# Kernel optimization log

Hardware: AMD Instinct MI355X
Metric: run time of the kernel (lower is better)

Reference implementation:

```python
import jax, jax.numpy as jnp
import numpy as np

B, N, H, NHEADS, N_COE, N_SCALES, THRE = 8, 1024, 128, 4, 50, 4, 5.0


def _layernorm(x, g, b, eps=1e-5):
    mu = x.mean(-1, keepdims=True)
    var = ((x - mu) ** 2).mean(-1, keepdims=True)
    return (x - mu) / jnp.sqrt(var + eps) * g + b


def setup_inputs() -> dict:
    key = jax.random.key(0)
    ks = jax.random.split(key, 12)

    def lin(k, out_d, in_d):
        lim = 1.0 / np.sqrt(in_d)
        kw, kb = jax.random.split(k)
        W = jax.random.uniform(kw, (out_d, in_d), minval=-lim, maxval=lim, dtype=jnp.float32)
        b = jax.random.uniform(kb, (out_d,), minval=-lim, maxval=lim, dtype=jnp.float32)
        return W, b

    eigw_W, eigw_b = lin(ks[0], H, H + 1)
    qkv_W, qkv_b = lin(ks[1], 3 * H, H)
    out_W, out_b = lin(ks[2], H, H)
    ffn1_W, ffn1_b = lin(ks[3], H, H)
    ffn2_W, ffn2_b = lin(ks[4], H, H)
    dsc_W, dsc_b = lin(ks[5], N_COE, H)
    dwav_W, dwav_b = lin(ks[6], N_COE, H)
    dscl_W, dscl_b = lin(ks[7], N_SCALES, H)
    # normalized-Laplacian eigenvalues live in [0, 2]
    eigenvalue = jax.random.uniform(ks[8], (B, N), minval=0.0, maxval=2.0, dtype=jnp.float32)
    eigenvector = jax.random.normal(ks[9], (B, N, N), dtype=jnp.float32) / np.sqrt(N)
    length = jnp.full((B,), N, dtype=jnp.int32)  # full graphs -> static shapes under jit
    return dict(
        eigenvalue=eigenvalue, eigenvector=eigenvector,
        eigw_W=eigw_W, eigw_b=eigw_b,
        ln1_g=jnp.ones((H,), jnp.float32), ln1_b=jnp.zeros((H,), jnp.float32),
        qkv_W=qkv_W, qkv_b=qkv_b, out_W=out_W, out_b=out_b,
        ln2_g=jnp.ones((H,), jnp.float32), ln2_b=jnp.zeros((H,), jnp.float32),
        ffn1_W=ffn1_W, ffn1_b=ffn1_b, ffn2_W=ffn2_W, ffn2_b=ffn2_b,
        dsc_W=dsc_W, dsc_b=dsc_b, dwav_W=dwav_W, dwav_b=dwav_b,
        dscl_W=dscl_W, dscl_b=dscl_b, length=length)


def _forward(eigenvalue, eigenvector, eigw_W, eigw_b, ln1_g, ln1_b, qkv_W, qkv_b,
             out_W, out_b, ln2_g, ln2_b, ffn1_W, ffn1_b, ffn2_W, ffn2_b,
             dsc_W, dsc_b, dwav_W, dwav_b, dscl_W, dscl_b, length):
    Bn, Nn = eigenvalue.shape
    mask1d = jnp.arange(Nn)[None, :] >= length[:, None]  # [B,N] True = padding

    # ---- SineEncoding ----
    ee = eigenvalue * 100.0
    div = jnp.exp(jnp.arange(0, H, 2, dtype=jnp.float32) * (-np.log(10000.0) / H))
    pe = ee[:, :, None] * div  # [B,N,H/2]
    eeig = jnp.concatenate([eigenvalue[:, :, None], jnp.sin(pe), jnp.cos(pe)], -1)  # [B,N,H+1]
    eig = eeig @ eigw_W.T + eigw_b  # [B,N,H]

    # ---- MHA block (pre-norm, residual) ----
    x = _layernorm(eig, ln1_g, ln1_b)
    qkv = x @ qkv_W.T + qkv_b
    q, k, v = jnp.split(qkv, 3, axis=-1)
    dh = H // NHEADS
    heads = lambda t: t.reshape(Bn, Nn, NHEADS, dh).transpose(0, 2, 1, 3)
    q, k, v = heads(q), heads(k), heads(v)
    scores = jnp.einsum('bhnd,bhmd->bhnm', q, k) / np.sqrt(dh)
    scores = jnp.where(mask1d[:, None, None, :], -1e9, scores)
    attn = jax.nn.softmax(scores, axis=-1)
    o = jnp.einsum('bhnm,bhmd->bhnd', attn, v).transpose(0, 2, 1, 3).reshape(Bn, Nn, H)
    eig = eig + (o @ out_W.T + out_b)

    # ---- FFN block (pre-norm, residual) ----
    y = _layernorm(eig, ln2_g, ln2_b)
    y = jax.nn.gelu(y @ ffn1_W.T + ffn1_b, approximate=False) @ ffn2_W.T + ffn2_b
    eig = eig + y

    # ---- decoders: masked mean-pool over eigenvalue axis ----
    len_f = length.astype(eig.dtype)[:, None] + 1e-8

    def pooled(W, b):
        c = eig @ W.T + b
        c = jnp.where(mask1d[:, :, None], 0.0, c)
        return c.sum(1) / len_f

    coe_scaling = jax.nn.sigmoid(pooled(dsc_W, dsc_b))          # [B,n_coe]
    coe_scaling = coe_scaling / (coe_scaling.sum(-1, keepdims=True) + 1e-8)
    coe_wavelet = jax.nn.sigmoid(pooled(dwav_W, dwav_b))        # [B,n_coe]
    coe_wavelet = coe_wavelet / (coe_wavelet.sum(-1, keepdims=True) + 1e-8)
    coe_scales = jax.nn.sigmoid(pooled(dscl_W, dscl_b)) * THRE  # [B,n_scales]

    # ---- Chebyshev-like recurrence (gen_base) via scan ----
    def gen_base(yv):
        te0, to0 = jnp.ones_like(yv), yv
        def step(carry, _):
            te, to = carry
            te = 2.0 * yv * to - te
            to = 2.0 * yv * te - to
            return (te, to), (te, to)
        _, (evens, odds) = jax.lax.scan(step, (te0, to0), None, length=N_COE - 1)
        wav = jnp.concatenate([te0[None], evens], 0)   # [n_coe, ...]
        scal = jnp.concatenate([to0[None], odds], 0)
        return scal, wav

    base_scaling, _ = gen_base(eigenvalue[:, :, None] - 1.0)  # [n_coe,B,N,1]
    fsw = eigenvalue[:, :, None] * coe_scales[:, None, :]     # [B,N,S]
    fsw = jnp.where(fsw > 2.0, 0.0, fsw)
    _, base_wavelet = gen_base(fsw - 1.0)                     # [n_coe,B,N,S]
    base_scaling = 0.5 * (1.0 - base_scaling)
    base_wavelet = 0.5 * (1.0 - base_wavelet)

    curr_scaling = jnp.einsum('bc,cbns->bns', coe_scaling, base_scaling)  # [B,N,1]
    curr_wavelet = jnp.einsum('bc,cbns->bns', coe_wavelet, base_wavelet)  # [B,N,S]
    fsa = jnp.concatenate([curr_scaling, curr_wavelet], -1)               # [B,N,S+1]
    # tight-frame normalization (cfg.lam.tight_use = True)
    fsa = fsa / (jnp.linalg.norm(fsa, axis=-1, keepdims=True) + 1e-8)

    # filters_i = evc @ diag(fsa[:,:,i]) @ evc^T, all scales at once
    filters = jnp.einsum('bnk,bks,bmk->bsnm', eigenvector, fsa, eigenvector)
    # F.normalize(filters) with default dim=1 -> normalize over row axis (n here)
    norm = jnp.sqrt(jnp.sum(filters ** 2, axis=2, keepdims=True))
    filters = filters / jnp.maximum(norm, 1e-12)
    # filters[edge_idx] with full lengths == flatten over (B,N,N), per scale
    bases = filters.transpose(1, 0, 2, 3).reshape(N_SCALES + 1, -1)
    return bases


def reference(eigenvalue, eigenvector, eigw_W, eigw_b, ln1_g, ln1_b, qkv_W, qkv_b,
              out_W, out_b, ln2_g, ln2_b, ffn1_W, ffn1_b, ffn2_W, ffn2_b,
              dsc_W, dsc_b, dwav_W, dwav_b, dscl_W, dscl_b, length):
    return _forward(eigenvalue, eigenvector, eigw_W, eigw_b, ln1_g, ln1_b, qkv_W, qkv_b,
                    out_W, out_b, ln2_g, ln2_b, ffn1_W, ffn1_b, ffn2_W, ffn2_b,
                    dsc_W, dsc_b, dwav_W, dwav_b, dscl_W, dscl_b, length)
```

## Files before the change

kernel.cpp:

```cpp
#include <hip/hip_runtime.h>
#include <hip/hip_bf16.h>
#include <cstdint>

#define BB 8
#define NV 1024
#define HH 128
#define DH 32
#define NCOE 50
#define NSC 4

#define WOFF_EIG 0
#define WOFF_QKV 16384
#define WOFF_OUT 65536
#define WOFF_F1  81920
#define WOFF_F2  98304
#define WB_ELEMS 114688

typedef __attribute__((ext_vector_type(8))) short short8;
typedef __attribute__((ext_vector_type(4))) float f32x4;

__device__ __forceinline__ ushort f2bf(float f) {
    uint32_t x = __float_as_uint(f);
    uint32_t r = x + 0x7FFFu + ((x >> 16) & 1u);
    return (ushort)(r >> 16);
}

#define GLDS(gp, lp) __builtin_amdgcn_global_load_lds((const __attribute__((address_space(1))) void*)(gp), (__attribute__((address_space(3))) void*)(lp), 16, 0, 0)

__global__ void k_wcvt(const float* __restrict__ eigw_W, const float* __restrict__ qkv_W,
                       const float* __restrict__ out_W, const float* __restrict__ f1W,
                       const float* __restrict__ f2W, ushort* __restrict__ Wb) {
    int idx = blockIdx.x * 256 + threadIdx.x;
    float v; int dst;
    if (idx < 16384) {
        int r = idx >> 7, k = idx & 127;
        v = eigw_W[r * 129 + 1 + k];
        dst = WOFF_EIG + (k >> 5) * 4096 + r * 32 + (k & 31);
    } else if (idx < 65536) {
        int l = idx - 16384; int c = l >> 14, rem = l & 16383;
        int r = rem >> 7, k = rem & 127;
        v = qkv_W[(size_t)(c * 128 + r) * 128 + k];
        dst = WOFF_QKV + c * 16384 + (k >> 5) * 4096 + r * 32 + (k & 31);
    } else if (idx < 81920) {
        int l = idx - 65536; int r = l >> 7, k = l & 127;
        v = out_W[r * 128 + k];
        dst = WOFF_OUT + (k >> 5) * 4096 + r * 32 + (k & 31);
    } else if (idx < 98304) {
        int l = idx - 81920; int r = l >> 7, k = l & 127;
        v = f1W[r * 128 + k];
        dst = WOFF_F1 + (k >> 5) * 4096 + r * 32 + (k & 31);
    } else {
        int l = idx - 98304; int r = l >> 7, k = l & 127;
        v = f2W[r * 128 + k];
        dst = WOFF_F2 + (k >> 5) * 4096 + r * 32 + (k & 31);
    }
    Wb[dst] = f2bf(v);
}

__global__ __launch_bounds__(256) void k_enc_sine(const float* __restrict__ ev, const ushort* __restrict__ Wb,
                                                  const float* __restrict__ eigw_W, const float* __restrict__ eigw_b,
                                                  float* __restrict__ eig) {
    __shared__ ushort As[16384];
    __shared__ ushort Bs[16384];
    int row0 = blockIdx.x * 128;
    int t = threadIdx.x, lane = t & 63, w = t >> 6;
    int wr = w >> 1, wc = w & 1;
#pragma unroll
    for (int p = 0; p < 8; ++p) {
        int ci = w * 8 + p;
        GLDS(Wb + WOFF_EIG + ci * 512 + lane * 8, Bs + ci * 512);
    }
    {
        int r = t >> 1, half = t & 1;
        float e = ev[row0 + r] * 100.0f;
#pragma unroll
        for (int ch = 0; ch < 8; ++ch) {
            short8 u;
#pragma unroll
            for (int l = 0; l < 8; ++l) {
                int j = ch * 8 + l;
                float div = expf((float)(2 * j) * -0.07195578415606394f);
                float pe = e * div;
                u[l] = (short)f2bf(half ? cosf(pe) : sinf(pe));
            }
            int k = half * 64 + ch * 8;
            *(short8*)(As + (k >> 5) * 4096 + r * 32 + (k & 31)) = u;
        }
    }
    __syncthreads();
    int cl = lane & 15, q = lane >> 4;
    f32x4 acc[4][4] = {};
#pragma unroll
    for (int kt = 0; kt < 4; ++kt) {
        const ushort* ap = As + kt * 4096 + (wr * 64 + cl) * 32 + q * 8;
        const ushort* bp = Bs + kt * 4096 + (wc * 64 + cl) * 32 + q * 8;
        short8 af[4], bfr[4];
#pragma unroll
        for (int i = 0; i < 4; ++i) af[i] = *(const short8*)(ap + i * 512);
#pragma unroll
        for (int j = 0; j < 4; ++j) bfr[j] = *(const short8*)(bp + j * 512);
#pragma unroll
        for (int i = 0; i < 4; ++i)
#pragma unroll
            for (int j = 0; j < 4; ++j)
                acc[i][j] = __builtin_amdgcn_mfma_f32_16x16x32_bf16(af[i], bfr[j], acc[i][j], 0, 0, 0);
    }
#pragma unroll
    for (int i = 0; i < 4; ++i) {
        int rbase = wr * 64 + i * 16 + q * 4;
        float er[4];
#pragma unroll
        for (int r = 0; r < 4; ++r) er[r] = ev[row0 + rbase + r];
#pragma unroll
        for (int j = 0; j < 4; ++j) {
            int col = wc * 64 + j * 16 + cl;
            float w0 = eigw_W[col * 129];
            float bv = eigw_b[col];
#pragma unroll
            for (int r = 0; r < 4; ++r)
                eig[(size_t)(row0 + rbase + r) * HH + col] = acc[i][j][r] + er[r] * w0 + bv;
        }
    }
}

__global__ __launch_bounds__(256) void k_enc_qkv(const float* __restrict__ eig, const float* __restrict__ g,
                                                 const float* __restrict__ be, const ushort* __restrict__ Wb,
                                                 const float* __restrict__ bias,
                                                 ushort* __restrict__ qb, ushort* __restrict__ kb, ushort* __restrict__ vb) {
    __shared__ ushort As[16384];
    __shared__ ushort Bs[16384];
    int row0 = blockIdx.x * 128;
    int t = threadIdx.x, lane = t & 63, w = t >> 6;
    int wr = w >> 1, wc = w & 1;
    {
        int r = t >> 1, half = t & 1;
        const float4* rowp = (const float4*)(eig + (size_t)(row0 + r) * HH + half * 64);
        float4 v[16];
        float s = 0.f, s2 = 0.f;
#pragma unroll
        for (int i = 0; i < 16; ++i) {
            float4 a = rowp[i]; v[i] = a;
            s += a.x + a.y + a.z + a.w;
            s2 += a.x * a.x + a.y * a.y + a.z * a.z + a.w * a.w;
        }
        s += __shfl_xor(s, 1); s2 += __shfl_xor(s2, 1);
        float mean = s * 0.0078125f;
        float var = s2 * 0.0078125f - mean * mean;
        float rstd = rsqrtf(var + 1e-5f);
        const float4* g4 = (const float4*)(g + half * 64);
        const float4* b4 = (const float4*)(be + half * 64);
#pragma unroll
        for (int ch = 0; ch < 8; ++ch) {
            float4 a = v[2 * ch], b2 = v[2 * ch + 1];
            float4 ga = g4[2 * ch], gb = g4[2 * ch + 1];
            float4 ba = b4[2 * ch], bb = b4[2 * ch + 1];
            short8 u;
            u[0] = (short)f2bf((a.x - mean) * rstd * ga.x + ba.x);
            u[1] = (short)f2bf((a.y - mean) * rstd * ga.y + ba.y);
            u[2] = (short)f2bf((a.z - mean) * rstd * ga.z + ba.z);
            u[3] = (short)f2bf((a.w - mean) * rstd * ga.w + ba.w);
            u[4] = (short)f2bf((b2.x - mean) * rstd * gb.x + bb.x);
            u[5] = (short)f2bf((b2.y - mean) * rstd * gb.y + bb.y);
            u[6] = (short)f2bf((b2.z - mean) * rstd * gb.z + bb.z);
            u[7] = (short)f2bf((b2.w - mean) * rstd * gb.w + bb.w);
            int k = half * 64 + ch * 8;
            *(short8*)(As + (k >> 5) * 4096 + r * 32 + (k & 31)) = u;
        }
    }
    int cl = lane & 15, q = lane >> 4;
    int bidx = row0 >> 10, nbase = row0 & (NV - 1);
    ushort* dsts[3] = {qb, kb, vb};
#pragma unroll 1
    for (int c = 0; c < 3; ++c) {
        __syncthreads();
#pragma unroll
        for (int p = 0; p < 8; ++p) {
            int ci = w * 8 + p;
            GLDS(Wb + WOFF_QKV + c * 16384 + ci * 512 + lane * 8, Bs + ci * 512);
        }
        __syncthreads();
        f32x4 acc[4][4] = {};
#pragma unroll
        for (int kt = 0; kt < 4; ++kt) {
            const ushort* ap = As + kt * 4096 + (wr * 64 + cl) * 32 + q * 8;
            const ushort* bp = Bs + kt * 4096 + (wc * 64 + cl) * 32 + q * 8;
            short8 af[4], bfr[4];
#pragma unroll
            for (int i = 0; i < 4; ++i) af[i] = *(const short8*)(ap + i * 512);
#pragma unroll
            for (int j = 0; j < 4; ++j) bfr[j] = *(const short8*)(bp + j * 512);
#pragma unroll
            for (int i = 0; i < 4; ++i)
#pragma unroll
                for (int j = 0; j < 4; ++j)
                    acc[i][j] = __builtin_amdgcn_mfma_f32_16x16x32_bf16(af[i], bfr[j], acc[i][j], 0, 0, 0);
        }
        ushort* dst = dsts[c];
#pragma unroll
        for (int j = 0; j < 4; ++j) {
            int col = wc * 64 + j * 16 + cl;
            float bv = bias[c * 128 + col];
            int h = col >> 5, dd = col & 31;
            ushort* hb = dst + ((size_t)(bidx * 4 + h) * NV + nbase) * DH + dd;
#pragma unroll
            for (int i = 0; i < 4; ++i) {
                int rbase = wr * 64 + i * 16 + q * 4;
#pragma unroll
                for (int r = 0; r < 4; ++r)
                    hb[(size_t)(rbase + r) * DH] = f2bf(acc[i][j][r] + bv);
            }
        }
    }
}

__global__ __launch_bounds__(256) void k_vt(const ushort* __restrict__ vb, ushort* __restrict__ vt) {
    __shared__ ushort Ld[256 * 40];
    int bh = blockIdx.y, n0 = blockIdx.x * 256;
    int t = threadIdx.x;
    const ushort* src = vb + ((size_t)bh * NV + n0) * DH;
#pragma unroll
    for (int p = 0; p < 4; ++p) {
        int idx = p * 256 + t;
        int rowi = idx >> 2, ch = idx & 3;
        short8 u = *(const short8*)(src + idx * 8);
        *(short8*)(&Ld[rowi * 40 + ch * 8]) = u;
    }
    __syncthreads();
    int d = t >> 3, nc = (t & 7) * 32;
    ushort* dst = vt + ((size_t)bh * DH + d) * NV + n0 + nc;
#pragma unroll
    for (int p = 0; p < 4; ++p) {
        short8 u;
#pragma unroll
        for (int i = 0; i < 8; ++i) u[i] = (short)Ld[(nc + p * 8 + i) * 40 + d];
        *(short8*)(dst + p * 8) = u;
    }
}

__global__ __launch_bounds__(256) void k_qk(const ushort* __restrict__ qb, const ushort* __restrict__ kb,
                                            float* __restrict__ S) {
    __shared__ ushort As[128 * 32];
    __shared__ ushort Bs[128 * 32];
    int tile = blockIdx.x;
    int bh = blockIdx.y;
    int n0 = (tile >> 3) * 128, m0 = (tile & 7) * 128;
    int tid = threadIdx.x, lane = tid & 63, w = tid >> 6;
    int wr = w >> 1, wc = w & 1;
    const ushort* qt = qb + ((size_t)bh * NV + n0) * DH;
    const ushort* ktb = kb + ((size_t)bh * NV + m0) * DH;
#pragma unroll
    for (int p = 0; p < 2; ++p) {
        int ci = w * 2 + p;
        GLDS(qt + ci * 512 + lane * 8, As + ci * 512);
        GLDS(ktb + ci * 512 + lane * 8, Bs + ci * 512);
    }
    __syncthreads();
    int cl = lane & 15, q = lane >> 4;
    const ushort* ap = As + ((wr * 64 + cl) * 32 + q * 8);
    const ushort* bp = Bs + ((wc * 64 + cl) * 32 + q * 8);
    short8 af[4], bfr[4];
#pragma unroll
    for (int i = 0; i < 4; ++i) af[i] = *(const short8*)(ap + i * 512);
#pragma unroll
    for (int j = 0; j < 4; ++j) bfr[j] = *(const short8*)(bp + j * 512);
    f32x4 acc[4][4] = {};
#pragma unroll
    for (int i = 0; i < 4; ++i)
#pragma unroll
        for (int j = 0; j < 4; ++j)
            acc[i][j] = __builtin_amdgcn_mfma_f32_16x16x32_bf16(af[i], bfr[j], acc[i][j], 0, 0, 0);
    size_t sb = (size_t)bh * NV * NV;
#pragma unroll
    for (int i = 0; i < 4; ++i) {
        int rbase = n0 + wr * 64 + i * 16 + q * 4;
#pragma unroll
        for (int j = 0; j < 4; ++j) {
            int col = m0 + wc * 64 + j * 16 + cl;
#pragma unroll
            for (int r = 0; r < 4; ++r)
                S[sb + (size_t)(rbase + r) * NV + col] = acc[i][j][r] * 0.17677669529663687f;
        }
    }
}

__global__ __launch_bounds__(256) void k_softmax(float* __restrict__ S) {
    __shared__ float red[4];
    int row = blockIdx.x, t = threadIdx.x, lane = t & 63;
    float* rp = S + (size_t)row * NV;
    float4 v = ((const float4*)rp)[t];
    float m = fmaxf(fmaxf(v.x, v.y), fmaxf(v.z, v.w));
#pragma unroll
    for (int off = 32; off; off >>= 1) m = fmaxf(m, __shfl_xor(m, off));
    if (lane == 0) red[t >> 6] = m;
    __syncthreads();
    m = fmaxf(fmaxf(red[0], red[1]), fmaxf(red[2], red[3]));
    __syncthreads();
    float e0 = __expf(v.x - m), e1 = __expf(v.y - m), e2 = __expf(v.z - m), e3 = __expf(v.w - m);
    float s4 = e0 + e1 + e2 + e3;
#pragma unroll
    for (int off = 32; off; off >>= 1) s4 += __shfl_xor(s4, off);
    if (lane == 0) red[t >> 6] = s4;
    __syncthreads();
    float inv = 1.0f / (red[0] + red[1] + red[2] + red[3]);
    ushort4 o;
    o.x = f2bf(e0 * inv); o.y = f2bf(e1 * inv); o.z = f2bf(e2 * inv); o.w = f2bf(e3 * inv);
    ((ushort4*)rp)[t] = o;
}

__global__ __launch_bounds__(256) void k_pv(const float* __restrict__ Sf, const ushort* __restrict__ vt,
                                            ushort* __restrict__ obuf) {
    __shared__ ushort As[128 * 32];
    __shared__ ushort Bs[32 * 32];
    int n0 = blockIdx.x * 128, bh = blockIdx.y;
    int b = bh >> 2, h = bh & 3;
    int tid = threadIdx.x, lane = tid & 63, w = tid >> 6;
    const char* Sb = (const char*)Sf;
    const ushort* vtb = vt + (size_t)bh * DH * NV;
    f32x4 acc[2][2] = {};
    for (int kt = 0; kt < NV / 32; ++kt) {
        int k0 = kt * 32;
        __syncthreads();
#pragma unroll
        for (int p = 0; p < 2; ++p) {
            int ci = w * 2 + p;
            int rrow = ci * 16 + (lane >> 2);
            int kch = (lane & 3) * 8;
            const ushort* gp = (const ushort*)(Sb + (size_t)(bh * NV + n0 + rrow) * 4096) + k0 + kch;
            GLDS(gp, As + ci * 512);
        }
        if (tid < 128) {
            int d = tid >> 2, ch = tid & 3;
            short8 u = *(const short8*)(vtb + (size_t)d * NV + k0 + ch * 8);
            *(short8*)(&Bs[d * 32 + ch * 8]) = u;
        }
        __syncthreads();
        int cl = lane & 15, q = lane >> 4;
        const ushort* ap = As + ((w * 32 + cl) * 32 + q * 8);
        const ushort* bp = Bs + (cl * 32 + q * 8);
        short8 af[2], bfr[2];
#pragma unroll
        for (int i = 0; i < 2; ++i) af[i] = *(const short8*)(ap + i * 512);
#pragma unroll
        for (int j = 0; j < 2; ++j) bfr[j] = *(const short8*)(bp + j * 512);
#pragma unroll
        for (int i = 0; i < 2; ++i)
#pragma unroll
            for (int j = 0; j < 2; ++j)
                acc[i][j] = __builtin_amdgcn_mfma_f32_16x16x32_bf16(af[i], bfr[j], acc[i][j], 0, 0, 0);
    }
    int cl = lane & 15, q = lane >> 4;
#pragma unroll
    for (int i = 0; i < 2; ++i) {
        int rbase = n0 + w * 32 + i * 16 + q * 4;
#pragma unroll
        for (int j = 0; j < 2; ++j) {
            int d = j * 16 + cl;
#pragma unroll
            for (int r = 0; r < 4; ++r)
                obuf[((size_t)(b * NV + rbase + r)) * HH + h * DH + d] = f2bf(acc[i][j][r]);
        }
    }
}

__global__ __launch_bounds__(256) void k_enc_proj(const ushort* __restrict__ obuf, const ushort* __restrict__ Wb,
                                                  const float* __restrict__ bias, float* __restrict__ eig) {
    __shared__ ushort As[16384];
    __shared__ ushort Bs[16384];
    int row0 = blockIdx.x * 128;
    int t = threadIdx.x, lane = t & 63, w = t >> 6;
    int wr = w >> 1, wc = w & 1;
#pragma unroll
    for (int p = 0; p < 8; ++p) {
        int ci = w * 8 + p;
        int kt = ci >> 3, rb = ci & 7;
        const ushort* gp = obuf + (size_t)(row0 + rb * 16 + (lane >> 2)) * HH + kt * 32 + (lane & 3) * 8;
        GLDS(gp, As + kt * 4096 + rb * 512);
        GLDS(Wb + WOFF_OUT + ci * 512 + lane * 8, Bs + ci * 512);
    }
    __syncthreads();
    int cl = lane & 15, q = lane >> 4;
    f32x4 acc[4][4] = {};
#pragma unroll
    for (int kt = 0; kt < 4; ++kt) {
        const ushort* ap = As + kt * 4096 + (wr * 64 + cl) * 32 + q * 8;
        const ushort* bp = Bs + kt * 4096 + (wc * 64 + cl) * 32 + q * 8;
        short8 af[4], bfr[4];
#pragma unroll
        for (int i = 0; i < 4; ++i) af[i] = *(const short8*)(ap + i * 512);
#pragma unroll
        for (int j = 0; j < 4; ++j) bfr[j] = *(const short8*)(bp + j * 512);
#pragma unroll
        for (int i = 0; i < 4; ++i)
#pragma unroll
            for (int j = 0; j < 4; ++j)
                acc[i][j] = __builtin_amdgcn_mfma_f32_16x16x32_bf16(af[i], bfr[j], acc[i][j], 0, 0, 0);
    }
#pragma unroll
    for (int j = 0; j < 4; ++j) {
        int col = wc * 64 + j * 16 + cl;
        float bv = bias[col];
#pragma unroll
        for (int i = 0; i < 4; ++i) {
            int rbase = wr * 64 + i * 16 + q * 4;
#pragma unroll
            for (int r = 0; r < 4; ++r) {
                size_t o = (size_t)(row0 + rbase + r) * HH + col;
                eig[o] += acc[i][j][r] + bv;
            }
        }
    }
}

__global__ __launch_bounds__(256) void k_enc_ffn(float* __restrict__ eig, const float* __restrict__ g,
                                                 const float* __restrict__ be, const ushort* __restrict__ Wb,
                                                 const float* __restrict__ b1, const float* __restrict__ b2) {
    __shared__ ushort As[16384];
    __shared__ ushort Bs[16384];
    int row0 = blockIdx.x * 128;
    int t = threadIdx.x, lane = t & 63, w = t >> 6;
    int wr = w >> 1, wc = w & 1;
    {
        int r = t >> 1, half = t & 1;
        const float4* rowp = (const float4*)(eig + (size_t)(row0 + r) * HH + half * 64);
        float4 v[16];
        float s = 0.f, s2 = 0.f;
#pragma unroll
        for (int i = 0; i < 16; ++i) {
            float4 a = rowp[i]; v[i] = a;
            s += a.x + a.y + a.z + a.w;
            s2 += a.x * a.x + a.y * a.y + a.z * a.z + a.w * a.w;
        }
        s += __shfl_xor(s, 1); s2 += __shfl_xor(s2, 1);
        float mean = s * 0.0078125f;
        float var = s2 * 0.0078125f - mean * mean;
        float rstd = rsqrtf(var + 1e-5f);
        const float4* g4 = (const float4*)(g + half * 64);
        const float4* b4 = (const float4*)(be + half * 64);
#pragma unroll
        for (int ch = 0; ch < 8; ++ch) {
            float4 a = v[2 * ch], bq = v[2 * ch + 1];
            float4 ga = g4[2 * ch], gb = g4[2 * ch + 1];
            float4 ba = b4[2 * ch], bb = b4[2 * ch + 1];
            short8 u;
            u[0] = (short)f2bf((a.x - mean) * rstd * ga.x + ba.x);
            u[1] = (short)f2bf((a.y - mean) * rstd * ga.y + ba.y);
            u[2] = (short)f2bf((a.z - mean) * rstd * ga.z + ba.z);
            u[3] = (short)f2bf((a.w - mean) * rstd * ga.w + ba.w);
            u[4] = (short)f2bf((bq.x - mean) * rstd * gb.x + bb.x);
            u[5] = (short)f2bf((bq.y - mean) * rstd * gb.y + bb.y);
            u[6] = (short)f2bf((bq.z - mean) * rstd * gb.z + bb.z);
            u[7] = (short)f2bf((bq.w - mean) * rstd * gb.w + bb.w);
            int k = half * 64 + ch * 8;
            *(short8*)(As + (k >> 5) * 4096 + r * 32 + (k & 31)) = u;
        }
    }
#pragma unroll
    for (int p = 0; p < 8; ++p) {
        int ci = w * 8 + p;
        GLDS(Wb + WOFF_F1 + ci * 512 + lane * 8, Bs + ci * 512);
    }
    __syncthreads();
    int cl = lane & 15, q = lane >> 4;
    f32x4 acc[4][4] = {};
#pragma unroll
    for (int kt = 0; kt < 4; ++kt) {
        const ushort* ap = As + kt * 4096 + (wr * 64 + cl) * 32 + q * 8;
        const ushort* bp = Bs + kt * 4096 + (wc * 64 + cl) * 32 + q * 8;
        short8 af[4], bfr[4];
#pragma unroll
        for (int i = 0; i < 4; ++i) af[i] = *(const short8*)(ap + i * 512);
#pragma unroll
        for (int j = 0; j < 4; ++j) bfr[j] = *(const short8*)(bp + j * 512);
#pragma unroll
        for (int i = 0; i < 4; ++i)
#pragma unroll
            for (int j = 0; j < 4; ++j)
                acc[i][j] = __builtin_amdgcn_mfma_f32_16x16x32_bf16(af[i], bfr[j], acc[i][j], 0, 0, 0);
    }
    __syncthreads();
#pragma unroll
    for (int j = 0; j < 4; ++j) {
        int col = wc * 64 + j * 16 + cl;
        float bv = b1[col];
        int koff = (col >> 5) * 4096 + (col & 31);
#pragma unroll
        for (int i = 0; i < 4; ++i) {
            int rbase = wr * 64 + i * 16 + q * 4;
#pragma unroll
            for (int r = 0; r < 4; ++r) {
                float a = acc[i][j][r] + bv;
                float ge = 0.5f * a * (1.0f + erff(a * 0.7071067811865475f));
                As[koff + (rbase + r) * 32] = f2bf(ge);
            }
        }
    }
#pragma unroll
    for (int p = 0; p < 8; ++p) {
        int ci = w * 8 + p;
        GLDS(Wb + WOFF_F2 + ci * 512 + lane * 8, Bs + ci * 512);
    }
    __syncthreads();
    f32x4 acc2[4][4] = {};
#pragma unroll
    for (int kt = 0; kt < 4; ++kt) {
        const ushort* ap = As + kt * 4096 + (wr * 64 + cl) * 32 + q * 8;
        const ushort* bp = Bs + kt * 4096 + (wc * 64 + cl) * 32 + q * 8;
        short8 af[4], bfr[4];
#pragma unroll
        for (int i = 0; i < 4; ++i) af[i] = *(const short8*)(ap + i * 512);
#pragma unroll
        for (int j = 0; j < 4; ++j) bfr[j] = *(const short8*)(bp + j * 512);
#pragma unroll
        for (int i = 0; i < 4; ++i)
#pragma unroll
            for (int j = 0; j < 4; ++j)
                acc2[i][j] = __builtin_amdgcn_mfma_f32_16x16x32_bf16(af[i], bfr[j], acc2[i][j], 0, 0, 0);
    }
#pragma unroll
    for (int j = 0; j < 4; ++j) {
        int col = wc * 64 + j * 16 + cl;
        float bv = b2[col];
#pragma unroll
        for (int i = 0; i < 4; ++i) {
            int rbase = wr * 64 + i * 16 + q * 4;
#pragma unroll
            for (int r = 0; r < 4; ++r) {
                size_t o = (size_t)(row0 + rbase + r) * HH + col;
                eig[o] += acc2[i][j][r] + bv;
            }
        }
    }
}

__global__ __launch_bounds__(1024) void k_meanpool(const float* __restrict__ eig, float* __restrict__ me) {
    __shared__ float part[8][HH];
    int b = blockIdx.x, t = threadIdx.x;
    int col = t & 127, grp = t >> 7;
    const float* p = eig + (size_t)b * NV * HH + (size_t)grp * 128 * HH + col;
    float s = 0.f;
    for (int n = 0; n < 128; ++n) s += p[(size_t)n * HH];
    part[grp][col] = s;
    __syncthreads();
    if (t < 128) {
        float a = 0.f;
#pragma unroll
        for (int g2 = 0; g2 < 8; ++g2) a += part[g2][t];
        me[b * HH + t] = a * (1.0f / NV);
    }
}

__global__ void k_decoders(const float* __restrict__ me,
                           const float* __restrict__ dscW, const float* __restrict__ dscb,
                           const float* __restrict__ dwavW, const float* __restrict__ dwavb,
                           const float* __restrict__ dsclW, const float* __restrict__ dsclb,
                           float* __restrict__ cs, float* __restrict__ cw, float* __restrict__ csc) {
    __shared__ float m[HH];
    __shared__ float s1[NCOE], s2[NCOE];
    __shared__ float sums[2];
    int b = blockIdx.x, t = threadIdx.x;
    m[t] = me[b * HH + t];
    m[t + 64] = me[b * HH + t + 64];
    __syncthreads();
    if (t < NCOE) {
        float a = dscb[t], a2 = dwavb[t];
        const float* w1 = dscW + t * HH;
        const float* w2 = dwavW + t * HH;
        for (int j = 0; j < HH; ++j) { a += m[j] * w1[j]; a2 += m[j] * w2[j]; }
        s1[t] = 1.f / (1.f + __expf(-a));
        s2[t] = 1.f / (1.f + __expf(-a2));
    }
    if (t < NSC) {
        float a = dsclb[t];
        const float* wv = dsclW + t * HH;
        for (int j = 0; j < HH; ++j) a += m[j] * wv[j];
        csc[b * NSC + t] = 5.0f / (1.f + __expf(-a));
    }
    __syncthreads();
    if (t == 0) {
        float a = 0.f, bb = 0.f;
        for (int c = 0; c < NCOE; ++c) { a += s1[c]; bb += s2[c]; }
        sums[0] = a; sums[1] = bb;
    }
    __syncthreads();
    if (t < NCOE) {
        cs[b * NCOE + t] = s1[t] / (sums[0] + 1e-8f);
        cw[b * NCOE + t] = s2[t] / (sums[1] + 1e-8f);
    }
}

__global__ void k_fsa(const float* __restrict__ ev, const float* __restrict__ cs,
                      const float* __restrict__ cw, const float* __restrict__ csc,
                      float* __restrict__ fsaT) {
    __shared__ float lcs[NCOE], lcw[NCOE], lsc[NSC];
    int gid = blockIdx.x * 256 + threadIdx.x;
    int b = gid >> 10, n = gid & (NV - 1);
    int t = threadIdx.x;
    if (t < NCOE) { lcs[t] = cs[b * NCOE + t]; lcw[t] = cw[b * NCOE + t]; }
    if (t < NSC) lsc[t] = csc[b * NSC + t];
    __syncthreads();
    float e = ev[gid];
    float x = e - 1.0f;
    float te = 1.f, to = x;
    float a0 = lcs[0] * 0.5f * (1.f - to);
    for (int c = 1; c < NCOE; ++c) {
        te = 2.f * x * to - te;
        to = 2.f * x * te - to;
        a0 += lcs[c] * 0.5f * (1.f - to);
    }
    float aw[NSC];
#pragma unroll
    for (int s = 0; s < NSC; ++s) {
        float f = e * lsc[s];
        if (f > 2.0f) f = 0.0f;
        float y = f - 1.0f;
        float te2 = 1.f, to2 = y, a = 0.f;
        for (int c = 1; c < NCOE; ++c) {
            te2 = 2.f * y * to2 - te2;
            to2 = 2.f * y * te2 - to2;
            a += lcw[c] * 0.5f * (1.f - te2);
        }
        aw[s] = a;
    }
    float n2 = a0 * a0;
#pragma unroll
    for (int s = 0; s < NSC; ++s) n2 += aw[s] * aw[s];
    float inv = 1.f / (sqrtf(n2) + 1e-8f);
    fsaT[((size_t)b * 5 + 0) * NV + n] = a0 * inv;
#pragma unroll
    for (int s = 0; s < NSC; ++s) fsaT[((size_t)b * 5 + 1 + s) * NV + n] = aw[s] * inv;
}

__global__ void k_tobf16(const float* __restrict__ in, ushort* __restrict__ outp) {
    int i = blockIdx.x * 256 + threadIdx.x;
    const float4* p = (const float4*)in + (size_t)i * 2;
    float4 a = p[0], bq = p[1];
    uint4 r;
    r.x = (uint)f2bf(a.x) | ((uint)f2bf(a.y) << 16);
    r.y = (uint)f2bf(a.z) | ((uint)f2bf(a.w) << 16);
    r.z = (uint)f2bf(bq.x) | ((uint)f2bf(bq.y) << 16);
    r.w = (uint)f2bf(bq.z) | ((uint)f2bf(bq.w) << 16);
    ((uint4*)outp)[i] = r;
}

__global__ __launch_bounds__(256) void k_gemm(const ushort* __restrict__ Vb,
                                              const float* __restrict__ fsaT,
                                              float* __restrict__ out,
                                              float* __restrict__ cn) {
    __shared__ ushort As[128 * 32];
    __shared__ ushort Bs[128 * 32];
    int tile = blockIdx.x;
    int bsid = blockIdx.y;
    int b = bsid / 5, s = bsid % 5;
    int n0 = (tile >> 3) * 128, m0 = (tile & 7) * 128;
    int tid = threadIdx.x, lane = tid & 63, w = tid >> 6;
    int wr = w >> 1, wc = w & 1;
    const ushort* Vbase = Vb + (size_t)b * NV * NV;
    const float* fs = fsaT + ((size_t)b * 5 + s) * NV;
    f32x4 acc[4][4] = {};

    for (int kt = 0; kt < NV / 32; ++kt) {
        int k0 = kt * 32;
        __syncthreads();
#pragma unroll
        for (int p = 0; p < 2; ++p) {
            int ci = w * 2 + p;
            int rrow = ci * 16 + (lane >> 2);
            int kch = (lane & 3) * 8;
            const ushort* gp = Vbase + (size_t)(m0 + rrow) * NV + k0 + kch;
            GLDS(gp, Bs + ci * 512);
        }
#pragma unroll
        for (int p = 0; p < 2; ++p) {
            int idx = p * 256 + tid;
            int rrow = idx >> 2;
            int kch = (idx & 3) * 8;
            const ushort* gp = Vbase + (size_t)(n0 + rrow) * NV + k0 + kch;
            uint4 raw = *(const uint4*)gp;
            const float4* fp = (const float4*)(fs + k0 + kch);
            float4 f0 = fp[0], f1 = fp[1];
            float v0 = __uint_as_float(raw.x << 16) * f0.x;
            float v1 = __uint_as_float(raw.x & 0xffff0000u) * f0.y;
            float v2 = __uint_as_float(raw.y << 16) * f0.z;
            float v3 = __uint_as_float(raw.y & 0xffff0000u) * f0.w;
            float v4 = __uint_as_float(raw.z << 16) * f1.x;
            float v5 = __uint_as_float(raw.z & 0xffff0000u) * f1.y;
            float v6 = __uint_as_float(raw.w << 16) * f1.z;
            float v7 = __uint_as_float(raw.w & 0xffff0000u) * f1.w;
            uint4 rr;
            rr.x = (uint)f2bf(v0) | ((uint)f2bf(v1) << 16);
            rr.y = (uint)f2bf(v2) | ((uint)f2bf(v3) << 16);
            rr.z = (uint)f2bf(v4) | ((uint)f2bf(v5) << 16);
            rr.w = (uint)f2bf(v6) | ((uint)f2bf(v7) << 16);
            *(uint4*)(As + rrow * 32 + kch) = rr;
        }
        __syncthreads();
        int cl = lane & 15, q = lane >> 4;
        const ushort* ap = As + ((wr * 64 + cl) * 32 + q * 8);
        const ushort* bp = Bs + ((wc * 64 + cl) * 32 + q * 8);
        short8 af[4], bfr[4];
#pragma unroll
        for (int i = 0; i < 4; ++i) af[i] = *(const short8*)(ap + i * 512);
#pragma unroll
        for (int j = 0; j < 4; ++j) bfr[j] = *(const short8*)(bp + j * 512);
#pragma unroll
        for (int i = 0; i < 4; ++i)
#pragma unroll
            for (int j = 0; j < 4; ++j)
                acc[i][j] = __builtin_amdgcn_mfma_f32_16x16x32_bf16(af[i], bfr[j], acc[i][j], 0, 0, 0);
    }
    int cl = lane & 15, q = lane >> 4;
    size_t ob = (size_t)(s * BB + b) * NV * NV;
    float colss[4] = {0.f, 0.f, 0.f, 0.f};
#pragma unroll
    for (int i = 0; i < 4; ++i) {
        int rbase = n0 + wr * 64 + i * 16 + q * 4;
#pragma unroll
        for (int j = 0; j < 4; ++j) {
            int col = m0 + wc * 64 + j * 16 + cl;
#pragma unroll
            for (int r = 0; r < 4; ++r) {
                float v = acc[i][j][r];
                out[ob + (size_t)(rbase + r) * NV + col] = v;
                colss[j] += v * v;
            }
        }
    }
    float* cnb = cn + (size_t)(s * BB + b) * NV;
#pragma unroll
    for (int j = 0; j < 4; ++j) {
        float v = colss[j];
        v += __shfl_xor(v, 16);
        v += __shfl_xor(v, 32);
        if (q == 0) atomicAdd(cnb + (m0 + wc * 64 + j * 16 + cl), v);
    }
}

__global__ void k_norm(float* __restrict__ out, const float* __restrict__ cn) {
    int bid = blockIdx.x;
    int bs = bid >> 10, n = bid & (NV - 1);
    int m4 = threadIdx.x * 4;
    float4 ssv = *(const float4*)(cn + (size_t)bs * NV + m4);
    float4* p = (float4*)(out + ((size_t)bs * NV + n) * NV + m4);
    float4 v = *p;
    v.x *= 1.f / fmaxf(sqrtf(ssv.x), 1e-12f);
    v.y *= 1.f / fmaxf(sqrtf(ssv.y), 1e-12f);
    v.z *= 1.f / fmaxf(sqrtf(ssv.z), 1e-12f);
    v.w *= 1.f / fmaxf(sqrtf(ssv.w), 1e-12f);
    *p = v;
}

extern "C" void kernel_launch(void* const* d_in, const int* in_sizes, int n_in,
                              void* d_out, int out_size, void* d_ws, size_t ws_size,
                              hipStream_t stream) {
    const float* eigenvalue = (const float*)d_in[0];
    const float* eigenvector = (const float*)d_in[1];
    const float* eigw_W = (const float*)d_in[2];
    const float* eigw_b = (const float*)d_in[3];
    const float* ln1_g = (const float*)d_in[4];
    const float* ln1_b = (const float*)d_in[5];
    const float* qkv_W = (const float*)d_in[6];
    const float* qkv_b = (const float*)d_in[7];
    const float* out_W = (const float*)d_in[8];
    const float* out_b = (const float*)d_in[9];
    const float* ln2_g = (const float*)d_in[10];
    const float* ln2_b = (const float*)d_in[11];
    const float* ffn1_W = (const float*)d_in[12];
    const float* ffn1_b = (const float*)d_in[13];
    const float* ffn2_W = (const float*)d_in[14];
    const float* ffn2_b = (const float*)d_in[15];
    const float* dsc_W = (const float*)d_in[16];
    const float* dsc_b = (const float*)d_in[17];
    const float* dwav_W = (const float*)d_in[18];
    const float* dwav_b = (const float*)d_in[19];
    const float* dscl_W = (const float*)d_in[20];
    const float* dscl_b = (const float*)d_in[21];

    char* w = (char*)d_ws;
    float* eig  = (float*)(w + 0);
    float* me   = (float*)(w + 4194304);
    float* cs   = (float*)(w + 4198400);
    float* cw   = (float*)(w + 4200448);
    float* csc  = (float*)(w + 4202496);
    float* fsaT = (float*)(w + 4203520);
    float* cn   = (float*)(w + 4367360);
    ushort* qb  = (ushort*)(w + 4531200);
    ushort* kb  = (ushort*)(w + 6628352);
    ushort* vb  = (ushort*)(w + 8725504);
    ushort* vt  = (ushort*)(w + 10822656);
    ushort* obuf = (ushort*)(w + 12919808);
    ushort* Wb  = (ushort*)(w + 15016960);
    ushort* Vb  = (ushort*)(w + 15246336);

    float* outp = (float*)d_out;
    float* S = (float*)d_out;

    hipMemsetAsync(cn, 0, 40 * NV * sizeof(float), stream);

    k_wcvt<<<dim3(WB_ELEMS / 256), dim3(256), 0, stream>>>(eigw_W, qkv_W, out_W, ffn1_W, ffn2_W, Wb);
    k_enc_sine<<<dim3(64), dim3(256), 0, stream>>>(eigenvalue, Wb, eigw_W, eigw_b, eig);
    k_enc_qkv<<<dim3(64), dim3(256), 0, stream>>>(eig, ln1_g, ln1_b, Wb, qkv_b, qb, kb, vb);
    k_vt<<<dim3(4, 32), dim3(256), 0, stream>>>(vb, vt);
    k_qk<<<dim3(64, 32), dim3(256), 0, stream>>>(qb, kb, S);
    k_softmax<<<dim3(32 * NV), dim3(256), 0, stream>>>(S);
    k_pv<<<dim3(8, 32), dim3(256), 0, stream>>>(S, vt, obuf);
    k_enc_proj<<<dim3(64), dim3(256), 0, stream>>>(obuf, Wb, out_b, eig);
    k_enc_ffn<<<dim3(64), dim3(256), 0, stream>>>(eig, ln2_g, ln2_b, Wb, ffn1_b, ffn2_b);
    k_meanpool<<<dim3(BB), dim3(1024), 0, stream>>>(eig, me);
    k_decoders<<<dim3(BB), dim3(64), 0, stream>>>(me, dsc_W, dsc_b, dwav_W, dwav_b, dscl_W, dscl_b, cs, cw, csc);
    k_fsa<<<dim3(BB * NV / 256), dim3(256), 0, stream>>>(eigenvalue, cs, cw, csc, fsaT);
    k_tobf16<<<dim3(BB * NV * NV / (8 * 256)), dim3(256), 0, stream>>>(eigenvector, Vb);
    k_gemm<<<dim3(64, 40), dim3(256), 0, stream>>>(Vb, fsaT, outp, cn);
    k_norm<<<dim3(40 * NV), dim3(256), 0, stream>>>(outp, cn);
}
```

Before: 565.6 us.

## Exploit filter symmetry with sqrt-prescaled operands and upper-triangle GEMM tiles

Each filter is V·diag(f)·V^T. The change folds sqrt(f) into a per-scale bf16 copy of the eigenvectors, so each filter becomes A·A^T. Only the 36 upper-triangular 128×128 tiles per (batch, scale) are computed, and each off-diagonal result is mirrored into the transposed location. Row and column sum-of-squares are accumulated for both halves. This roughly halves the MFMA work, but adds a prescale pass that writes about 80MB of scaled operands and makes the mirrored stores strided. It also assumes the filter coefficients are nonnegative, and it runs only when the workspace is large enough.

```diff
diff --git a/kernel.cpp b/kernel.cpp
--- a/kernel.cpp
+++ b/kernel.cpp
@@ -590,7 +590,7 @@
 
 __global__ void k_fsa(const float* __restrict__ ev, const float* __restrict__ cs,
                       const float* __restrict__ cw, const float* __restrict__ csc,
-                      float* __restrict__ fsaT) {
+                      float* __restrict__ fsaT, float* __restrict__ fsqT) {
     __shared__ float lcs[NCOE], lcw[NCOE], lsc[NSC];
     int gid = blockIdx.x * 256 + threadIdx.x;
     int b = gid >> 10, n = gid & (NV - 1);
@@ -625,9 +625,15 @@
 #pragma unroll
     for (int s = 0; s < NSC; ++s) n2 += aw[s] * aw[s];
     float inv = 1.f / (sqrtf(n2) + 1e-8f);
-    fsaT[((size_t)b * 5 + 0) * NV + n] = a0 * inv;
-#pragma unroll
-    for (int s = 0; s < NSC; ++s) fsaT[((size_t)b * 5 + 1 + s) * NV + n] = aw[s] * inv;
+    float v0 = a0 * inv;
+    fsaT[((size_t)b * 5 + 0) * NV + n] = v0;
+    if (fsqT) fsqT[((size_t)b * 5 + 0) * NV + n] = sqrtf(fmaxf(v0, 0.f));
+#pragma unroll
+    for (int s = 0; s < NSC; ++s) {
+        float vs = aw[s] * inv;
+        fsaT[((size_t)b * 5 + 1 + s) * NV + n] = vs;
+        if (fsqT) fsqT[((size_t)b * 5 + 1 + s) * NV + n] = sqrtf(fmaxf(vs, 0.f));
+    }
 }
 
 __global__ void k_tobf16(const float* __restrict__ in, ushort* __restrict__ outp) {
@@ -640,6 +646,118 @@
     r.z = (uint)f2bf(bq.x) | ((uint)f2bf(bq.y) << 16);
     r.w = (uint)f2bf(bq.z) | ((uint)f2bf(bq.w) << 16);
     ((uint4*)outp)[i] = r;
+}
+
+__global__ __launch_bounds__(256) void k_prescale(const float* __restrict__ evec, const float* __restrict__ fsq,
+                                                  ushort* __restrict__ Asc) {
+    int gid = blockIdx.x * 256 + threadIdx.x;
+    int gk = gid & 127;
+    int n = (gid >> 7) & (NV - 1);
+    int b = gid >> 17;
+    const float4* vp = (const float4*)(evec + ((size_t)b * NV + n) * NV + gk * 8);
+    float4 a = vp[0], c = vp[1];
+    int gsw = (gk & ~3) | ((gk ^ (n >> 2)) & 3);
+    size_t dstbase = ((size_t)(b * 5) * NV + n) * NV + (size_t)gsw * 8;
+#pragma unroll
+    for (int s = 0; s < 5; ++s) {
+        const float* fp = fsq + (size_t)(b * 5 + s) * NV + gk * 8;
+        float4 f0 = *(const float4*)fp, f1 = *(const float4*)(fp + 4);
+        uint4 r;
+        r.x = (uint)f2bf(a.x * f0.x) | ((uint)f2bf(a.y * f0.y) << 16);
+        r.y = (uint)f2bf(a.z * f0.z) | ((uint)f2bf(a.w * f0.w) << 16);
+        r.z = (uint)f2bf(c.x * f1.x) | ((uint)f2bf(c.y * f1.y) << 16);
+        r.w = (uint)f2bf(c.z * f1.z) | ((uint)f2bf(c.w * f1.w) << 16);
+        *(uint4*)(Asc + dstbase + (size_t)s * NV * NV) = r;
+    }
+}
+
+__global__ __launch_bounds__(256) void k_gemm_sym(const ushort* __restrict__ Asc,
+                                                  float* __restrict__ out,
+                                                  float* __restrict__ cn) {
+    __shared__ ushort As[128 * 32];
+    __shared__ ushort Bs[128 * 32];
+    int lin = blockIdx.x;
+    int wg = (lin & 7) * 180 + (lin >> 3);
+    int bs = wg / 36, p = wg % 36;
+    int b = bs / 5, s = bs % 5;
+    int ti = 0, rem = p;
+    while (rem >= 8 - ti) { rem -= 8 - ti; ++ti; }
+    int tj = ti + rem;
+    int n0 = ti * 128, m0 = tj * 128;
+    int tid = threadIdx.x, lane = tid & 63, w = tid >> 6;
+    int wr = w >> 1, wc = w & 1;
+    const ushort* Abase = Asc + (size_t)(b * 5 + s) * NV * NV;
+    int cl = lane & 15, q = lane >> 4;
+    int qx = (q ^ (cl >> 2)) & 3;
+    int fo = cl * 32 + qx * 8;
+    f32x4 acc[4][4] = {};
+    for (int kt = 0; kt < NV / 32; ++kt) {
+        int k0 = kt * 32;
+        __syncthreads();
+#pragma unroll
+        for (int p2 = 0; p2 < 2; ++p2) {
+            int ci = w * 2 + p2;
+            int rrow = ci * 16 + (lane >> 2);
+            int kch = (lane & 3) * 8;
+            GLDS(Abase + (size_t)(n0 + rrow) * NV + k0 + kch, As + ci * 512);
+            GLDS(Abase + (size_t)(m0 + rrow) * NV + k0 + kch, Bs + ci * 512);
+        }
+        __syncthreads();
+        short8 af[4], bfr[4];
+#pragma unroll
+        for (int i = 0; i < 4; ++i) af[i] = *(const short8*)(As + (wr * 4 + i) * 512 + fo);
+#pragma unroll
+        for (int j = 0; j < 4; ++j) bfr[j] = *(const short8*)(Bs + (wc * 4 + j) * 512 + fo);
+#pragma unroll
+        for (int i = 0; i < 4; ++i)
+#pragma unroll
+            for (int j = 0; j < 4; ++j)
+                acc[i][j] = __builtin_amdgcn_mfma_f32_16x16x32_bf16(af[i], bfr[j], acc[i][j], 0, 0, 0);
+    }
+    size_t ob = (size_t)(s * BB + b) * NV * NV;
+    float* cnb = cn + (size_t)(s * BB + b) * NV;
+    float colss[4] = {0.f, 0.f, 0.f, 0.f};
+    float rowss[4][4];
+#pragma unroll
+    for (int i = 0; i < 4; ++i)
+#pragma unroll
+        for (int r = 0; r < 4; ++r) rowss[i][r] = 0.f;
+#pragma unroll
+    for (int i = 0; i < 4; ++i) {
+        int rbase = n0 + wr * 64 + i * 16 + q * 4;
+#pragma unroll
+        for (int j = 0; j < 4; ++j) {
+            int col = m0 + wc * 64 + j * 16 + cl;
+            float4 tv;
+#pragma unroll
+            for (int r = 0; r < 4; ++r) {
+                float v = acc[i][j][r];
+                out[ob + (size_t)(rbase + r) * NV + col] = v;
+                colss[j] += v * v;
+                rowss[i][r] += v * v;
+                ((float*)&tv)[r] = v;
+            }
+            if (ti != tj) *(float4*)(out + ob + (size_t)col * NV + rbase) = tv;
+        }
+    }
+#pragma unroll
+    for (int j = 0; j < 4; ++j) {
+        float v = colss[j];
+        v += __shfl_xor(v, 16);
+        v += __shfl_xor(v, 32);
+        if (q == 0) atomicAdd(cnb + (m0 + wc * 64 + j * 16 + cl), v);
+    }
+    if (ti != tj) {
+#pragma unroll
+        for (int i = 0; i < 4; ++i)
+#pragma unroll
+            for (int r = 0; r < 4; ++r) {
+                float v = rowss[i][r];
+                v += __shfl_xor(v, 1); v += __shfl_xor(v, 2);
+                v += __shfl_xor(v, 4); v += __shfl_xor(v, 8);
+                if (cl == 0) atomicAdd(cnb + (n0 + wr * 64 + i * 16 + q * 4 + r), v);
+            }
+    }
 }
 
 __global__ __launch_bounds__(256) void k_gemm(const ushort* __restrict__ Vb,
@@ -791,6 +909,10 @@
     ushort* Wb  = (ushort*)(w + 15016960);
     ushort* Vb  = (ushort*)(w + 15246336);
 
+    bool big = ws_size >= (size_t)117440512;
+    float* fsqT = big ? (float*)(w + 32023552) : nullptr;
+    ushort* Asc = (ushort*)(w + 33554432);
+
     float* outp = (float*)d_out;
     float* S = (float*)d_out;
 
@@ -807,8 +929,13 @@
     k_enc_ffn<<<dim3(64), dim3(256), 0, stream>>>(eig, ln2_g, ln2_b, Wb, ffn1_b, ffn2_b);
     k_meanpool<<<dim3(BB), dim3(1024), 0, stream>>>(eig, me);
     k_decoders<<<dim3(BB), dim3(64), 0, stream>>>(me, dsc_W, dsc_b, dwav_W, dwav_b, dscl_W, dscl_b, cs, cw, csc);
-    k_fsa<<<dim3(BB * NV / 256), dim3(256), 0, stream>>>(eigenvalue, cs, cw, csc, fsaT);
-    k_tobf16<<<dim3(BB * NV * NV / (8 * 256)), dim3(256), 0, stream>>>(eigenvector, Vb);
-    k_gemm<<<dim3(64, 40), dim3(256), 0, stream>>>(Vb, fsaT, outp, cn);
+    k_fsa<<<dim3(BB * NV / 256), dim3(256), 0, stream>>>(eigenvalue, cs, cw, csc, fsaT, fsqT);
+    if (big) {
+        k_prescale<<<dim3(BB * NV * 128 / 256), dim3(256), 0, stream>>>(eigenvector, fsqT, Asc);
+        k_gemm_sym<<<dim3(36 * 40), dim3(256), 0, stream>>>(Asc, outp, cn);
+    } else {
+        k_tobf16<<<dim3(BB * NV * NV / (8 * 256)), dim3(256), 0, stream>>>(eigenvector, Vb);
+        k_gemm<<<dim3(64, 40), dim3(256), 0, stream>>>(Vb, fsaT, outp, cn);
+    }
     k_norm<<<dim3(40 * NV), dim3(256), 0, stream>>>(outp, cn);
 }
```

After: 525.4 us. 1.08x faster.
